# Kernel optimization log

Measured on AMD Instinct MI355X. Metric: run time of the kernel, lower is better.

The kernel has to match this reference:

```python
import jax, jax.numpy as jnp
import numpy as np

N = 10000       # atoms
E = 160000      # edges
F = 128         # node_dim
NB = 20         # num radial basis
BLOCKS = 3      # action_blocks
CUTOFF = 5.0
ZMAX = 100
EPS = 1e-8


def _layernorm(x, g, b):
    mu = jnp.mean(x, axis=-1, keepdims=True)
    var = jnp.var(x, axis=-1, keepdims=True)
    return (x - mu) * jax.lax.rsqrt(var + 1e-5) * g + b


def setup_inputs() -> dict:
    key = jax.random.key(0)
    ks = jax.random.split(key, 16)
    W = 0.05  # weight init scale, keeps activations stable over 3 blocks
    inp = {
        "pos": jax.random.uniform(ks[0], (N, 3), dtype=jnp.float32),
        "z": jax.random.randint(ks[1], (N,), 0, ZMAX),
        "edge_index": jax.random.randint(ks[2], (2, E), 0, N),
        "z_embed": jax.random.normal(ks[3], (ZMAX, F), dtype=jnp.float32),
        "Wrbf": jax.random.normal(ks[4], (BLOCKS, NB, 3 * F), dtype=jnp.float32) * W,
        "brbf": jnp.zeros((BLOCKS, 3 * F), jnp.float32),
        "ln_g": jnp.ones((BLOCKS, F), jnp.float32),
        "ln_b": jnp.zeros((BLOCKS, F), jnp.float32),
        "Wm1": jax.random.normal(ks[5], (BLOCKS, F, F), dtype=jnp.float32) * W,
        "bm1": jnp.zeros((BLOCKS, F), jnp.float32),
        "Wm2": jax.random.normal(ks[6], (BLOCKS, F, 3 * F), dtype=jnp.float32) * W,
        "bm2": jnp.zeros((BLOCKS, 3 * F), jnp.float32),
        "Uw": jax.random.normal(ks[7], (BLOCKS, F, F), dtype=jnp.float32) * W,
        "Vw": jax.random.normal(ks[8], (BLOCKS, F, F), dtype=jnp.float32) * W,
        "ln2_g": jnp.ones((BLOCKS, F), jnp.float32),
        "ln2_b": jnp.zeros((BLOCKS, F), jnp.float32),
        "Wu1": jax.random.normal(ks[9], (BLOCKS, 2 * F, F), dtype=jnp.float32) * W,
        "bu1": jnp.zeros((BLOCKS, F), jnp.float32),
        "Wu2": jax.random.normal(ks[10], (BLOCKS, F, 3 * F), dtype=jnp.float32) * W,
        "bu2": jnp.zeros((BLOCKS, 3 * F), jnp.float32),
        "Wo1": jax.random.normal(ks[11], (F, F), dtype=jnp.float32) * W,
        "bo1": jnp.zeros((F,), jnp.float32),
        "Wo2": jax.random.normal(ks[12], (F, 1), dtype=jnp.float32) * W,
        "bo2": jnp.zeros((1,), jnp.float32),
    }
    return inp


def _forward(pos, z, edge_index, z_embed, Wrbf, brbf, ln_g, ln_b, Wm1, bm1,
             Wm2, bm2, Uw, Vw, ln2_g, ln2_b, Wu1, bu1, Wu2, bu2,
             Wo1, bo1, Wo2, bo2):
    src, dst = edge_index[0], edge_index[1]
    # ---- edge data: distances, bessel RBF, cosine cutoff ----
    rvec = pos[dst] - pos[src]                          # [E,3]
    d = jnp.sqrt(jnp.sum(rvec * rvec, axis=-1) + EPS)   # [E]
    rhat = rvec / d[:, None]                            # [E,3]
    n = jnp.arange(1, NB + 1, dtype=jnp.float32)
    rbf = jnp.sin(n[None, :] * jnp.pi * d[:, None] / CUTOFF) / d[:, None]  # [E,NB]
    fc = jnp.where(d < CUTOFF, 0.5 * (jnp.cos(jnp.pi * d / CUTOFF) + 1.0), 0.0)
    # ---- embedding ----
    x = z_embed[z]                                      # [N,F] scalar features
    v = jnp.zeros((x.shape[0], 3, F), x.dtype)          # [N,3,F] vector features
    nseg = x.shape[0]
    for b in range(BLOCKS):
        # ---- message block (PaiNN) ----
        xn = _layernorm(x, ln_g[b], ln_b[b])
        phi = jax.nn.silu(xn @ Wm1[b] + bm1[b]) @ Wm2[b] + bm2[b]          # [N,3F]
        Wf = (rbf @ Wrbf[b] + brbf[b]) * fc[:, None]                       # [E,3F]
        m = phi[src] * Wf                                                  # [E,3F]
        ms, mvv, mvs = m[:, :F], m[:, F:2 * F], m[:, 2 * F:]
        dx = jax.ops.segment_sum(ms, dst, num_segments=nseg)               # [N,F]
        ev = mvv[:, None, :] * v[src] + mvs[:, None, :] * rhat[:, :, None] # [E,3,F]
        dv = jax.ops.segment_sum(ev, dst, num_segments=nseg)               # [N,3,F]
        x = x + dx
        v = v + dv
        # ---- update block (PaiNN) ----
        Uv = jnp.einsum('ncf,fg->ncg', v, Uw[b])
        Vv = jnp.einsum('ncf,fg->ncg', v, Vw[b])
        vnorm = jnp.sqrt(jnp.sum(Vv * Vv, axis=1) + EPS)                   # [N,F]
        xn2 = _layernorm(x, ln2_g[b], ln2_b[b])
        a = jax.nn.silu(jnp.concatenate([xn2, vnorm], -1) @ Wu1[b] + bu1[b]) @ Wu2[b] + bu2[b]
        avv, asv, ass = a[:, :F], a[:, F:2 * F], a[:, 2 * F:]
        x = x + asv * jnp.sum(Uv * Vv, axis=1) + ass
        v = v + avv[:, None, :] * Uv
    # ---- energy output head ----
    e_atom = jax.nn.silu(x @ Wo1 + bo1) @ Wo2 + bo2                        # [N,1]
    return jnp.sum(e_atom)


def reference(pos, z, edge_index, z_embed, Wrbf, brbf, ln_g, ln_b, Wm1, bm1,
              Wm2, bm2, Uw, Vw, ln2_g, ln2_b, Wu1, bu1, Wu2, bu2,
              Wo1, bo1, Wo2, bo2):
    return _forward(pos, z, edge_index, z_embed, Wrbf, brbf, ln_g, ln_b,
                    Wm1, bm1, Wm2, bm2, Uw, Vw, ln2_g, ln2_b,
                    Wu1, bu1, Wu2, bu2, Wo1, bo1, Wo2, bo2)
```

## Files before the change

kernel.cpp:

```cpp
#include <hip/hip_runtime.h>
#include <math.h>

#define N_ATOM 10000
#define NEDGE  160000
#define F      128
#define F3     384
#define NB     20
#define NBLK   3
#define PI_F   3.14159265358979323846f

typedef __attribute__((ext_vector_type(8))) short bf16x8;
typedef __attribute__((ext_vector_type(4))) float f32x4;
#define MFMA16(a,b,c) __builtin_amdgcn_mfma_f32_16x16x32_bf16(a,b,c,0,0,0)

__device__ __forceinline__ float silu_f(float x){ return x / (1.0f + __expf(-x)); }
__device__ __forceinline__ short f2b(float f){
  unsigned u = __float_as_uint(f);
  u += 0x7fff + ((u >> 16) & 1);
  return (short)(u >> 16);
}
__device__ __forceinline__ float b2f(short s){
  return __uint_as_float(((unsigned)(unsigned short)s) << 16);
}

__global__ __launch_bounds__(256) void k_prep(const float* __restrict__ Wm1, const float* __restrict__ Wm2,
                                              const float* __restrict__ Uw,  const float* __restrict__ Vw,
                                              const float* __restrict__ Wu1, const float* __restrict__ Wu2,
                                              short* __restrict__ wt){
  int idx = blockIdx.x * 256 + threadIdx.x;
  short* wm1t = wt;
  short* wm2t = wt + 49152;
  short* uwt  = wt + 196608;
  short* vwt  = wt + 245760;
  short* wu1t = wt + 294912;
  short* wu2t = wt + 393216;
  if (idx < 49152){
    int b = idx >> 14, r = idx & 16383, n = r >> 7, k = r & 127;
    wm1t[idx] = f2b(Wm1[b*16384 + k*128 + n]);
  } else if (idx < 196608){
    int j = idx - 49152;
    int b = j / 49152, r = j % 49152, n = r >> 7, k = r & 127;
    wm2t[j] = f2b(Wm2[b*49152 + k*384 + n]);
  } else if (idx < 245760){
    int j = idx - 196608;
    int b = j >> 14, r = j & 16383, n = r >> 7, k = r & 127;
    uwt[j] = f2b(Uw[b*16384 + k*128 + n]);
  } else if (idx < 294912){
    int j = idx - 245760;
    int b = j >> 14, r = j & 16383, n = r >> 7, k = r & 127;
    vwt[j] = f2b(Vw[b*16384 + k*128 + n]);
  } else if (idx < 393216){
    int j = idx - 294912;
    int b = j >> 15, r = j & 32767, n = r >> 8, k = r & 255;
    wu1t[j] = f2b(Wu1[b*32768 + k*128 + n]);
  } else if (idx < 540672){
    int j = idx - 393216;
    int b = j / 49152, r = j % 49152, n = r >> 7, k = r & 127;
    wu2t[j] = f2b(Wu2[b*49152 + k*384 + n]);
  }
}

__global__ __launch_bounds__(256) void k_init(const float* __restrict__ z_embed,
                                              const int* __restrict__ z,
                                              float* __restrict__ x, float* __restrict__ v){
  int idx = blockIdx.x * 256 + threadIdx.x;
  if (idx < N_ATOM * F){
    int i = idx >> 7, f = idx & 127;
    x[idx] = z_embed[z[i] * F + f];
  }
  if (idx < N_ATOM * 3 * F) v[idx] = 0.0f;
}

__global__ __launch_bounds__(256) void k_hist(const int* __restrict__ ei, int* __restrict__ deg){
  int e = blockIdx.x * 256 + threadIdx.x;
  atomicAdd(&deg[ei[NEDGE + e]], 1);
}

__global__ __launch_bounds__(1024) void k_scan(const int* __restrict__ deg,
                                               int* __restrict__ rowptr, int* __restrict__ cursor){
  __shared__ int part[1024];
  int t = threadIdx.x;
  int base = t * 10;
  int loc[10];
  int s = 0;
  #pragma unroll
  for (int i = 0; i < 10; i++){
    int idx = base + i;
    int d = (idx < N_ATOM) ? deg[idx] : 0;
    loc[i] = s; s += d;
  }
  part[t] = s;
  __syncthreads();
  for (int off = 1; off < 1024; off <<= 1){
    int vp = 0;
    if (t >= off) vp = part[t - off];
    __syncthreads();
    part[t] += vp;
    __syncthreads();
  }
  int offset = (t == 0) ? 0 : part[t - 1];
  #pragma unroll
  for (int i = 0; i < 10; i++){
    int idx = base + i;
    if (idx < N_ATOM){ rowptr[idx] = offset + loc[i]; cursor[idx] = offset + loc[i]; }
  }
  if (t == 1023) rowptr[N_ATOM] = part[1023];
}

__global__ __launch_bounds__(256) void k_slot(const int* __restrict__ ei,
                                              int* __restrict__ cursor, int* __restrict__ slot){
  int e = blockIdx.x * 256 + threadIdx.x;
  int p = atomicAdd(&cursor[ei[NEDGE + e]], 1);
  slot[e] = p;
}

__global__ __launch_bounds__(256) void k_geo(const float* __restrict__ pos,
                                             const int* __restrict__ ei,
                                             const int* __restrict__ slot,
                                             int* __restrict__ srcs,
                                             float* __restrict__ rhs,
                                             float* __restrict__ rbfs,
                                             float* __restrict__ fcs){
  int e = blockIdx.x * 256 + threadIdx.x;
  int s = ei[e], d_ = ei[NEDGE + e];
  int p = slot[e];
  float rx = pos[d_*3+0] - pos[s*3+0];
  float ry = pos[d_*3+1] - pos[s*3+1];
  float rz = pos[d_*3+2] - pos[s*3+2];
  float d  = sqrtf(rx*rx + ry*ry + rz*rz + 1e-8f);
  float inv = 1.0f / d;
  srcs[p] = s;
  rhs[p*3+0] = rx*inv; rhs[p*3+1] = ry*inv; rhs[p*3+2] = rz*inv;
  float fcv = (d < 5.0f) ? 0.5f * (cosf(PI_F * d * 0.2f) + 1.0f) : 0.0f;
  fcs[p] = fcv;
  float base = PI_F * d * 0.2f;
  float sc = inv * fcv;
  #pragma unroll
  for (int k = 0; k < NB; k++){
    rbfs[(size_t)p*NB + k] = sinf(base * (float)(k+1)) * sc;
  }
}

__global__ __launch_bounds__(256) void k_node_phi(const float* __restrict__ x,
                                                  float* __restrict__ phi,
                                                  const float* __restrict__ ln_g, const float* __restrict__ ln_b,
                                                  const short* __restrict__ Wm1t, const float* __restrict__ bm1,
                                                  const short* __restrict__ Wm2t, const float* __restrict__ bm2){
  __shared__ short xn_s[64*136];
  __shared__ short h_s [64*136];
  __shared__ float mu_s[64], rs_s[64];
  int t = threadIdx.x;
  int row0 = blockIdx.x * 64; if (row0 > N_ATOM - 64) row0 = N_ATOM - 64;

  {
    int r = t >> 2, q = t & 3;
    const float* xr = x + (size_t)(row0 + r) * F;
    float s = 0.f, ss = 0.f;
    #pragma unroll
    for (int i = 0; i < 32; i++){ float vv = xr[q + 4*i]; s += vv; ss += vv*vv; }
    s += __shfl_xor(s, 1, 64); ss += __shfl_xor(ss, 1, 64);
    s += __shfl_xor(s, 2, 64); ss += __shfl_xor(ss, 2, 64);
    if (q == 0){
      float mu = s * (1.0f/F);
      mu_s[r] = mu; rs_s[r] = rsqrtf(ss * (1.0f/F) - mu*mu + 1e-5f);
    }
  }
  __syncthreads();
  #pragma unroll
  for (int i = 0; i < 32; i++){
    int idx = t + 256*i; int r = idx >> 7, f = idx & 127;
    float vv = x[(size_t)(row0 + r)*F + f];
    xn_s[r*136 + f] = f2b((vv - mu_s[r]) * rs_s[r] * ln_g[f] + ln_b[f]);
  }
  __syncthreads();

  int l = t & 63, w = t >> 6;
  int wr0  = w * 16;
  int arow = wr0 + (l & 15);
  int kof  = (l >> 4) * 8;
  int drow = wr0 + (l >> 4) * 4;

  {
    bf16x8 af[4];
    #pragma unroll
    for (int ks = 0; ks < 4; ks++) af[ks] = *(const bf16x8*)&xn_s[arow*136 + ks*32 + kof];
    #pragma unroll
    for (int ct = 0; ct < 8; ct++){
      int col = ct*16 + (l & 15);
      float bb = bm1[col];
      f32x4 acc = {bb, bb, bb, bb};
      #pragma unroll
      for (int ks = 0; ks < 4; ks++){
        bf16x8 bf = *(const bf16x8*)&Wm1t[col*F + ks*32 + kof];
        acc = MFMA16(af[ks], bf, acc);
      }
      #pragma unroll
      for (int i = 0; i < 4; i++) h_s[(drow + i)*136 + col] = f2b(silu_f(acc[i]));
    }
  }
  __syncthreads();
  {
    bf16x8 af[4];
    #pragma unroll
    for (int ks = 0; ks < 4; ks++) af[ks] = *(const bf16x8*)&h_s[arow*136 + ks*32 + kof];
    #pragma unroll
    for (int ct = 0; ct < 24; ct++){
      int col = ct*16 + (l & 15);
      float bb = bm2[col];
      f32x4 acc = {bb, bb, bb, bb};
      #pragma unroll
      for (int ks = 0; ks < 4; ks++){
        bf16x8 bf = *(const bf16x8*)&Wm2t[col*F + ks*32 + kof];
        acc = MFMA16(af[ks], bf, acc);
      }
      #pragma unroll
      for (int i = 0; i < 4; i++) phi[(size_t)(row0 + drow + i)*F3 + col] = acc[i];
    }
  }
}

__global__ __launch_bounds__(256) void k_edge_g(const int* __restrict__ rowptr,
                                                const int* __restrict__ srcs,
                                                const float* __restrict__ rbfs,
                                                const float* __restrict__ rhs,
                                                const float* __restrict__ fcs,
                                                const float* __restrict__ phi,
                                                const float* __restrict__ v,
                                                const float* __restrict__ Wrbf,
                                                const float* __restrict__ brbf,
                                                float* __restrict__ x,
                                                float* __restrict__ vnew){
  __shared__ float W[NB * F3];
  int t = threadIdx.x;
  #pragma unroll
  for (int i = 0; i < (NB*F3)/256; i++) W[t + 256*i] = Wrbf[t + 256*i];
  __syncthreads();

  int wid = t >> 6, lane = t & 63;
  int n = blockIdx.x * 4 + wid;
  int f0 = lane, f1 = lane + 64;
  int r0 = rowptr[n], r1 = rowptr[n+1];

  float bs0  = brbf[f0],       bs1  = brbf[f1];
  float bvv0 = brbf[F + f0],   bvv1 = brbf[F + f1];
  float bvs0 = brbf[2*F + f0], bvs1 = brbf[2*F + f1];

  float ax0=0.f, ax1=0.f;
  float av00=0.f, av01=0.f, av10=0.f, av11=0.f, av20=0.f, av21=0.f;

  for (int j = r0; j < r1; ++j){
    int s = srcs[j];
    float fcv = fcs[j];
    float rh0 = rhs[j*3+0], rh1 = rhs[j*3+1], rh2 = rhs[j*3+2];
    const float* rb = rbfs + (size_t)j * NB;
    float w_s0=0.f, w_s1=0.f, wvv0=0.f, wvv1=0.f, wvs0=0.f, wvs1=0.f;
    #pragma unroll
    for (int k = 0; k < NB; k++){
      float r = rb[k];
      w_s0 += r * W[k*F3 + f0];        w_s1 += r * W[k*F3 + f1];
      wvv0 += r * W[k*F3 + F + f0];    wvv1 += r * W[k*F3 + F + f1];
      wvs0 += r * W[k*F3 + 2*F + f0];  wvs1 += r * W[k*F3 + 2*F + f1];
    }
    const float* ps = phi + (size_t)s * F3;
    const float* vs = v   + (size_t)s * 3 * F;
    float ms0  = ps[f0]       * (w_s0 + bs0 *fcv);
    float ms1  = ps[f1]       * (w_s1 + bs1 *fcv);
    float mvv0 = ps[F + f0]   * (wvv0 + bvv0*fcv);
    float mvv1 = ps[F + f1]   * (wvv1 + bvv1*fcv);
    float mvs0 = ps[2*F + f0] * (wvs0 + bvs0*fcv);
    float mvs1 = ps[2*F + f1] * (wvs1 + bvs1*fcv);
    ax0 += ms0; ax1 += ms1;
    av00 += mvv0*vs[f0]       + mvs0*rh0;  av01 += mvv1*vs[f1]       + mvs1*rh0;
    av10 += mvv0*vs[F + f0]   + mvs0*rh1;  av11 += mvv1*vs[F + f1]   + mvs1*rh1;
    av20 += mvv0*vs[2*F + f0] + mvs0*rh2;  av21 += mvv1*vs[2*F + f1] + mvs1*rh2;
  }

  size_t xb = (size_t)n * F;
  x[xb + f0] += ax0;  x[xb + f1] += ax1;
  size_t vb = (size_t)n * 3 * F;
  vnew[vb + f0]       = v[vb + f0]       + av00;  vnew[vb + f1]       = v[vb + f1]       + av01;
  vnew[vb + F + f0]   = v[vb + F + f0]   + av10;  vnew[vb + F + f1]   = v[vb + F + f1]   + av11;
  vnew[vb + 2*F + f0] = v[vb + 2*F + f0] + av20;  vnew[vb + 2*F + f1] = v[vb + 2*F + f1] + av21;
}

__global__ __launch_bounds__(256) void k_node_upd(float* __restrict__ x, float* __restrict__ v,
                                                  const float* __restrict__ vnew,
                                                  const short* __restrict__ Uwt, const short* __restrict__ Vwt,
                                                  const float* __restrict__ ln2_g, const float* __restrict__ ln2_b,
                                                  const short* __restrict__ Wu1t, const float* __restrict__ bu1,
                                                  const short* __restrict__ Wu2t, const float* __restrict__ bu2){
  __shared__ __align__(16) char smem[59776];
  short* vt   = (short*)smem;
  short* Uv_s = (short*)(smem + 13056);
  char*  R    = smem + 26112;
  short* Vv_s = (short*)R;
  short* ab   = (short*)(R + 13056);
  float* a_s  = (float*)R;
  short* h2   = (short*)(smem + 50688);
  short* duv  = (short*)(smem + 55040);
  float* mu_s = (float*)(smem + 59392);
  float* rs_s = mu_s + 16;

  int t = threadIdx.x;
  int n0 = blockIdx.x * 16;

  {
    int r = t >> 4, q = t & 15;
    const float* xr = x + (size_t)(n0 + r) * F;
    float s = 0.f, ss = 0.f;
    #pragma unroll
    for (int i = 0; i < 8; i++){ float vv = xr[q + 16*i]; s += vv; ss += vv*vv; }
    #pragma unroll
    for (int m = 8; m >= 1; m >>= 1){ s += __shfl_xor(s, m, 64); ss += __shfl_xor(ss, m, 64); }
    if (q == 0){ float mu = s*(1.0f/F); mu_s[r] = mu; rs_s[r] = rsqrtf(ss*(1.0f/F) - mu*mu + 1e-5f); }
  }
  #pragma unroll
  for (int i = 0; i < 24; i++){
    int idx = t + 256*i; int row = idx >> 7, f = idx & 127;
    vt[row*136 + f] = f2b(vnew[(size_t)(n0*3 + row)*F + f]);
  }
  __syncthreads();

  int l = t & 63, w = t >> 6;
  int kof = (l >> 4) * 8;

  {
    #pragma unroll
    for (int jj = 0; jj < 3; jj++){
      int job = w*3 + jj;
      int rt = job >> 2, rem = job & 3, mat = rem >> 1, ch = rem & 1;
      const short* Bt = mat ? Vwt : Uwt;
      short* Out = mat ? Vv_s : Uv_s;
      bf16x8 af[4];
      #pragma unroll
      for (int ks = 0; ks < 4; ks++) af[ks] = *(const bf16x8*)&vt[(rt*16 + (l&15))*136 + ks*32 + kof];
      #pragma unroll
      for (int ct = 0; ct < 4; ct++){
        int col = ch*64 + ct*16 + (l & 15);
        f32x4 acc = {0.f, 0.f, 0.f, 0.f};
        #pragma unroll
        for (int ks = 0; ks < 4; ks++){
          bf16x8 bf = *(const bf16x8*)&Bt[col*F + ks*32 + kof];
          acc = MFMA16(af[ks], bf, acc);
        }
        #pragma unroll
        for (int i = 0; i < 4; i++) Out[(rt*16 + (l>>4)*4 + i)*136 + col] = f2b(acc[i]);
      }
    }
  }
  __syncthreads();

  {
    #pragma unroll
    for (int i = 0; i < 8; i++){
      int idx = t + 256*i; int n = idx >> 7, f = idx & 127;
      float xv = x[(size_t)(n0 + n)*F + f];
      ab[n*264 + f] = f2b((xv - mu_s[n]) * rs_s[n] * ln2_g[f] + ln2_b[f]);
      float v0 = b2f(Vv_s[(3*n+0)*136 + f]), v1 = b2f(Vv_s[(3*n+1)*136 + f]), v2 = b2f(Vv_s[(3*n+2)*136 + f]);
      float u0 = b2f(Uv_s[(3*n+0)*136 + f]), u1 = b2f(Uv_s[(3*n+1)*136 + f]), u2 = b2f(Uv_s[(3*n+2)*136 + f]);
      ab[n*264 + 128 + f] = f2b(sqrtf(v0*v0 + v1*v1 + v2*v2 + 1e-8f));
      duv[n*136 + f] = f2b(u0*v0 + u1*v1 + u2*v2);
    }
  }
  __syncthreads();

  {
    bf16x8 af[8];
    #pragma unroll
    for (int ks = 0; ks < 8; ks++) af[ks] = *(const bf16x8*)&ab[(l&15)*264 + ks*32 + kof];
    #pragma unroll
    for (int cc = 0; cc < 2; cc++){
      int col = (w*2 + cc)*16 + (l & 15);
      float bb = bu1[col];
      f32x4 acc = {bb, bb, bb, bb};
      #pragma unroll
      for (int ks = 0; ks < 8; ks++){
        bf16x8 bf = *(const bf16x8*)&Wu1t[col*256 + ks*32 + kof];
        acc = MFMA16(af[ks], bf, acc);
      }
      #pragma unroll
      for (int i = 0; i < 4; i++) h2[((l>>4)*4 + i)*136 + col] = f2b(silu_f(acc[i]));
    }
  }
  __syncthreads();

  {
    bf16x8 af[4];
    #pragma unroll
    for (int ks = 0; ks < 4; ks++) af[ks] = *(const bf16x8*)&h2[(l&15)*136 + ks*32 + kof];
    #pragma unroll
    for (int cc = 0; cc < 6; cc++){
      int col = (w*6 + cc)*16 + (l & 15);
      float bb = bu2[col];
      f32x4 acc = {bb, bb, bb, bb};
      #pragma unroll
      for (int ks = 0; ks < 4; ks++){
        bf16x8 bf = *(const bf16x8*)&Wu2t[col*F + ks*32 + kof];
        acc = MFMA16(af[ks], bf, acc);
      }
      #pragma unroll
      for (int i = 0; i < 4; i++) a_s[((l>>4)*4 + i)*384 + col] = acc[i];
    }
  }
  __syncthreads();

  {
    #pragma unroll
    for (int i = 0; i < 8; i++){
      int idx = t + 256*i; int n = idx >> 7, f = idx & 127;
      float avv = a_s[n*384 + f], asv = a_s[n*384 + 128 + f], ass = a_s[n*384 + 256 + f];
      size_t xr_ = (size_t)(n0 + n)*F + f;
      x[xr_] = x[xr_] + asv * b2f(duv[n*136 + f]) + ass;
      #pragma unroll
      for (int c = 0; c < 3; c++){
        size_t vr = (size_t)((n0 + n)*3 + c)*F + f;
        v[vr] = vnew[vr] + avv * b2f(Uv_s[(3*n + c)*136 + f]);
      }
    }
  }
}

__global__ __launch_bounds__(256) void k_out(const float* __restrict__ x,
                                             const float* __restrict__ Wo1, const float* __restrict__ bo1,
                                             const float* __restrict__ Wo2, const float* __restrict__ bo2,
                                             float* __restrict__ out){
  __shared__ float xl[8][F];
  __shared__ float hl[8][F];
  __shared__ float er[8];
  int t = threadIdx.x; int n0 = blockIdx.x * 8;
  #pragma unroll
  for (int i = 0; i < 4; i++){ int idx = t + 256*i; ((float*)xl)[idx] = x[(size_t)n0*F + idx]; }
  __syncthreads();
  { int g = t & 127, grp = t >> 7;
    float acc[4];
    #pragma unroll
    for (int n = 0; n < 4; n++) acc[n] = bo1[g];
    for (int k = 0; k < F; k++){
      float w = Wo1[k*F + g];
      #pragma unroll
      for (int n = 0; n < 4; n++) acc[n] += xl[grp*4+n][k] * w;
    }
    #pragma unroll
    for (int n = 0; n < 4; n++) hl[grp*4+n][g] = silu_f(acc[n]);
  }
  __syncthreads();
  { int r = t >> 5, lq = t & 31;
    float s = 0.f;
    #pragma unroll
    for (int i = 0; i < 4; i++) s += hl[r][lq + 32*i] * Wo2[lq + 32*i];
    #pragma unroll
    for (int m = 16; m >= 1; m >>= 1) s += __shfl_xor(s, m, 64);
    if (lq == 0) er[r] = s + bo2[0];
  }
  __syncthreads();
  if (t == 0){
    float s = 0.f;
    #pragma unroll
    for (int r = 0; r < 8; r++) s += er[r];
    unsafeAtomicAdd(out, s);
  }
}

extern "C" void kernel_launch(void* const* d_in, const int* in_sizes, int n_in,
                              void* d_out, int out_size, void* d_ws, size_t ws_size,
                              hipStream_t stream){
  const float* pos     = (const float*)d_in[0];
  const int*   z       = (const int*)  d_in[1];
  const int*   ei      = (const int*)  d_in[2];
  const float* z_embed = (const float*)d_in[3];
  const float* Wrbf    = (const float*)d_in[4];
  const float* brbf    = (const float*)d_in[5];
  const float* ln_g    = (const float*)d_in[6];
  const float* ln_b    = (const float*)d_in[7];
  const float* Wm1     = (const float*)d_in[8];
  const float* bm1     = (const float*)d_in[9];
  const float* Wm2     = (const float*)d_in[10];
  const float* bm2     = (const float*)d_in[11];
  const float* Uw      = (const float*)d_in[12];
  const float* Vw      = (const float*)d_in[13];
  const float* ln2_g   = (const float*)d_in[14];
  const float* ln2_b   = (const float*)d_in[15];
  const float* Wu1     = (const float*)d_in[16];
  const float* bu1     = (const float*)d_in[17];
  const float* Wu2     = (const float*)d_in[18];
  const float* bu2     = (const float*)d_in[19];
  const float* Wo1     = (const float*)d_in[20];
  const float* bo1     = (const float*)d_in[21];
  const float* Wo2     = (const float*)d_in[22];
  const float* bo2     = (const float*)d_in[23];

  float* ws = (float*)d_ws;
  size_t o = 0;
  float* x     = ws + o; o += (size_t)N_ATOM * F;
  float* v     = ws + o; o += (size_t)N_ATOM * 3 * F;
  float* phi   = ws + o; o += (size_t)N_ATOM * 3 * F;
  float* vnew  = ws + o; o += (size_t)N_ATOM * 3 * F;
  float* rhs   = ws + o; o += (size_t)NEDGE * 3;
  float* rbfs  = ws + o; o += (size_t)NEDGE * NB;
  float* fcs   = ws + o; o += (size_t)NEDGE;
  int*   rowptr= (int*)(ws + o); o += N_ATOM + 16;
  int*   srcs  = (int*)(ws + o); o += NEDGE;
  short* wt    = (short*)(ws + o); o += 270336 + 8;
  int* deg    = (int*)vnew;
  int* cursor = deg + 10240;
  int* slot   = cursor + 10240;

  short* wm1t = wt;
  short* wm2t = wt + 49152;
  short* uwt  = wt + 196608;
  short* vwt  = wt + 245760;
  short* wu1t = wt + 294912;
  short* wu2t = wt + 393216;

  hipMemsetAsync(d_out, 0, sizeof(float), stream);
  hipMemsetAsync(deg, 0, N_ATOM * sizeof(int), stream);
  k_prep<<<2112, 256, 0, stream>>>(Wm1, Wm2, Uw, Vw, Wu1, Wu2, wt);
  k_hist<<<NEDGE/256, 256, 0, stream>>>(ei, deg);
  k_scan<<<1, 1024, 0, stream>>>(deg, rowptr, cursor);
  k_slot<<<NEDGE/256, 256, 0, stream>>>(ei, cursor, slot);
  k_geo <<<NEDGE/256, 256, 0, stream>>>(pos, ei, slot, srcs, rhs, rbfs, fcs);
  k_init<<<(N_ATOM*3*F + 255)/256, 256, 0, stream>>>(z_embed, z, x, v);

  for (int b = 0; b < NBLK; b++){
    k_node_phi<<<157, 256, 0, stream>>>(x, phi,
        ln_g + b*F, ln_b + b*F, wm1t + b*16384, bm1 + b*F,
        wm2t + b*49152, bm2 + b*F3);
    k_edge_g<<<N_ATOM/4, 256, 0, stream>>>(rowptr, srcs, rbfs, rhs, fcs,
        phi, v, Wrbf + (size_t)b*NB*F3, brbf + b*F3, x, vnew);
    k_node_upd<<<N_ATOM/16, 256, 0, stream>>>(x, v, vnew,
        uwt + b*16384, vwt + b*16384,
        ln2_g + b*F, ln2_b + b*F,
        wu1t + b*32768, bu1 + b*F,
        wu2t + b*49152, bu2 + b*F3);
  }
  k_out<<<N_ATOM/8, 256, 0, stream>>>(x, Wo1, bo1, Wo2, bo2, (float*)d_out);
}
```

Baseline: 689.8 us.

## Store phi and v in packed bf16 for edge gather, retile node_phi to 16 rows

The per-edge gathers of phi and v now read bf16-packed copies, with phi written packed straight from the MLP and v packed by a new small kernel each block. This halves the bytes fetched per edge in the gather-bound message kernel. k_node_phi is retiled to 16 rows per block with the waves splitting output columns, giving many more blocks. The message kernel now writes only the delta dv, and the update kernel adds v+dv itself. The cost is an extra pack kernel and bf16 rounding of gathered features.

```diff
diff --git a/kernel.cpp b/kernel.cpp
--- a/kernel.cpp
+++ b/kernel.cpp
@@ -21,6 +21,11 @@
 }
 __device__ __forceinline__ float b2f(short s){
   return __uint_as_float(((unsigned)(unsigned short)s) << 16);
+}
+__device__ __forceinline__ float blo(unsigned u){ return __uint_as_float(u << 16); }
+__device__ __forceinline__ float bhi(unsigned u){ return __uint_as_float(u & 0xffff0000u); }
+__device__ __forceinline__ unsigned packb(float a, float b){
+  return ((unsigned)(unsigned short)f2b(a)) | (((unsigned)(unsigned short)f2b(b)) << 16);
 }
 
 __global__ __launch_bounds__(256) void k_prep(const float* __restrict__ Wm1, const float* __restrict__ Wm2,
@@ -71,6 +76,12 @@
   if (idx < N_ATOM * 3 * F) v[idx] = 0.0f;
 }
 
+__global__ __launch_bounds__(256) void k_packv(const float* __restrict__ v, unsigned* __restrict__ v_b){
+  int idx = blockIdx.x * 256 + threadIdx.x;
+  const float* p = v + (size_t)idx * 2;
+  v_b[idx] = packb(p[0], p[1]);
+}
+
 __global__ __launch_bounds__(256) void k_hist(const int* __restrict__ ei, int* __restrict__ deg){
   int e = blockIdx.x * 256 + threadIdx.x;
   atomicAdd(&deg[ei[NEDGE + e]], 1);
@@ -142,24 +153,24 @@
 }
 
 __global__ __launch_bounds__(256) void k_node_phi(const float* __restrict__ x,
-                                                  float* __restrict__ phi,
+                                                  unsigned* __restrict__ phi_b,
                                                   const float* __restrict__ ln_g, const float* __restrict__ ln_b,
                                                   const short* __restrict__ Wm1t, const float* __restrict__ bm1,
                                                   const short* __restrict__ Wm2t, const float* __restrict__ bm2){
-  __shared__ short xn_s[64*136];
-  __shared__ short h_s [64*136];
-  __shared__ float mu_s[64], rs_s[64];
+  __shared__ short xn_s[16*136];
+  __shared__ short h_s [16*136];
+  __shared__ float mu_s[16], rs_s[16];
   int t = threadIdx.x;
-  int row0 = blockIdx.x * 64; if (row0 > N_ATOM - 64) row0 = N_ATOM - 64;
-
-  {
-    int r = t >> 2, q = t & 3;
+  int row0 = blockIdx.x * 16;
+
+  {
+    int r = t >> 4, q = t & 15;
     const float* xr = x + (size_t)(row0 + r) * F;
     float s = 0.f, ss = 0.f;
     #pragma unroll
-    for (int i = 0; i < 32; i++){ float vv = xr[q + 4*i]; s += vv; ss += vv*vv; }
-    s += __shfl_xor(s, 1, 64); ss += __shfl_xor(ss, 1, 64);
-    s += __shfl_xor(s, 2, 64); ss += __shfl_xor(ss, 2, 64);
+    for (int i = 0; i < 8; i++){ float vv = xr[q + 16*i]; s += vv; ss += vv*vv; }
+    #pragma unroll
+    for (int m = 8; m >= 1; m >>= 1){ s += __shfl_xor(s, m, 64); ss += __shfl_xor(ss, m, 64); }
     if (q == 0){
       float mu = s * (1.0f/F);
       mu_s[r] = mu; rs_s[r] = rsqrtf(ss * (1.0f/F) - mu*mu + 1e-5f);
@@ -167,7 +178,7 @@
   }
   __syncthreads();
   #pragma unroll
-  for (int i = 0; i < 32; i++){
+  for (int i = 0; i < 8; i++){
     int idx = t + 256*i; int r = idx >> 7, f = idx & 127;
     float vv = x[(size_t)(row0 + r)*F + f];
     xn_s[r*136 + f] = f2b((vv - mu_s[r]) * rs_s[r] * ln_g[f] + ln_b[f]);
@@ -175,18 +186,16 @@
   __syncthreads();
 
   int l = t & 63, w = t >> 6;
-  int wr0  = w * 16;
-  int arow = wr0 + (l & 15);
-  int kof  = (l >> 4) * 8;
-  int drow = wr0 + (l >> 4) * 4;
+  int kof = (l >> 4) * 8;
+  int arow = l & 15;
 
   {
     bf16x8 af[4];
     #pragma unroll
     for (int ks = 0; ks < 4; ks++) af[ks] = *(const bf16x8*)&xn_s[arow*136 + ks*32 + kof];
     #pragma unroll
-    for (int ct = 0; ct < 8; ct++){
-      int col = ct*16 + (l & 15);
+    for (int cc = 0; cc < 2; cc++){
+      int col = (w*2 + cc)*16 + (l & 15);
       float bb = bm1[col];
       f32x4 acc = {bb, bb, bb, bb};
       #pragma unroll
@@ -195,26 +204,34 @@
         acc = MFMA16(af[ks], bf, acc);
       }
       #pragma unroll
-      for (int i = 0; i < 4; i++) h_s[(drow + i)*136 + col] = f2b(silu_f(acc[i]));
-    }
-  }
-  __syncthreads();
-  {
-    bf16x8 af[4];
-    #pragma unroll
-    for (int ks = 0; ks < 4; ks++) af[ks] = *(const bf16x8*)&h_s[arow*136 + ks*32 + kof];
-    #pragma unroll
-    for (int ct = 0; ct < 24; ct++){
-      int col = ct*16 + (l & 15);
+      for (int i = 0; i < 4; i++) h_s[((l>>4)*4 + i)*136 + col] = f2b(silu_f(acc[i]));
+    }
+  }
+  __syncthreads();
+  {
+    bf16x8 ah[4];
+    #pragma unroll
+    for (int ks = 0; ks < 4; ks++) ah[ks] = *(const bf16x8*)&h_s[arow*136 + ks*32 + kof];
+    #pragma unroll
+    for (int cc = 0; cc < 6; cc++){
+      int col = (w*6 + cc)*16 + (l & 15);
       float bb = bm2[col];
       f32x4 acc = {bb, bb, bb, bb};
       #pragma unroll
       for (int ks = 0; ks < 4; ks++){
         bf16x8 bf = *(const bf16x8*)&Wm2t[col*F + ks*32 + kof];
-        acc = MFMA16(af[ks], bf, acc);
-      }
-      #pragma unroll
-      for (int i = 0; i < 4; i++) phi[(size_t)(row0 + drow + i)*F3 + col] = acc[i];
+        acc = MFMA16(ah[ks], bf, acc);
+      }
+      #pragma unroll
+      for (int i = 0; i < 4; i++){
+        float val = acc[i];
+        float oth = __shfl_xor(val, 1, 64);
+        if (!(l & 1)){
+          int row = row0 + (l>>4)*4 + i;
+          int seg = col >> 7, cin = col & 127;
+          phi_b[(size_t)row*192 + seg*64 + (cin >> 1)] = packb(val, oth);
+        }
+      }
     }
   }
 }
@@ -224,12 +241,12 @@
                                                 const float* __restrict__ rbfs,
                                                 const float* __restrict__ rhs,
                                                 const float* __restrict__ fcs,
-                                                const float* __restrict__ phi,
-                                                const float* __restrict__ v,
+                                                const unsigned* __restrict__ phi_b,
+                                                const unsigned* __restrict__ v_b,
                                                 const float* __restrict__ Wrbf,
                                                 const float* __restrict__ brbf,
                                                 float* __restrict__ x,
-                                                float* __restrict__ vnew){
+                                                float* __restrict__ dv){
   __shared__ float W[NB * F3];
   int t = threadIdx.x;
   #pragma unroll
@@ -238,53 +255,58 @@
 
   int wid = t >> 6, lane = t & 63;
   int n = blockIdx.x * 4 + wid;
-  int f0 = lane, f1 = lane + 64;
+  int f0 = 2 * lane;
   int r0 = rowptr[n], r1 = rowptr[n+1];
 
-  float bs0  = brbf[f0],       bs1  = brbf[f1];
-  float bvv0 = brbf[F + f0],   bvv1 = brbf[F + f1];
-  float bvs0 = brbf[2*F + f0], bvs1 = brbf[2*F + f1];
+  float2 bs  = *(const float2*)&brbf[f0];
+  float2 bvv = *(const float2*)&brbf[F + f0];
+  float2 bvs = *(const float2*)&brbf[2*F + f0];
 
   float ax0=0.f, ax1=0.f;
   float av00=0.f, av01=0.f, av10=0.f, av11=0.f, av20=0.f, av21=0.f;
 
   for (int j = r0; j < r1; ++j){
     int s = srcs[j];
+    const unsigned* pb = phi_b + (size_t)s * 192 + lane;
+    const unsigned* vb = v_b   + (size_t)s * 192 + lane;
+    unsigned p0 = pb[0], p1 = pb[64], p2 = pb[128];
+    unsigned q0 = vb[0], q1 = vb[64], q2 = vb[128];
     float fcv = fcs[j];
     float rh0 = rhs[j*3+0], rh1 = rhs[j*3+1], rh2 = rhs[j*3+2];
     const float* rb = rbfs + (size_t)j * NB;
-    float w_s0=0.f, w_s1=0.f, wvv0=0.f, wvv1=0.f, wvs0=0.f, wvs1=0.f;
+    float ws0=0.f, ws1=0.f, wv0=0.f, wv1=0.f, wq0=0.f, wq1=0.f;
     #pragma unroll
     for (int k = 0; k < NB; k++){
       float r = rb[k];
-      w_s0 += r * W[k*F3 + f0];        w_s1 += r * W[k*F3 + f1];
-      wvv0 += r * W[k*F3 + F + f0];    wvv1 += r * W[k*F3 + F + f1];
-      wvs0 += r * W[k*F3 + 2*F + f0];  wvs1 += r * W[k*F3 + 2*F + f1];
-    }
-    const float* ps = phi + (size_t)s * F3;
-    const float* vs = v   + (size_t)s * 3 * F;
-    float ms0  = ps[f0]       * (w_s0 + bs0 *fcv);
-    float ms1  = ps[f1]       * (w_s1 + bs1 *fcv);
-    float mvv0 = ps[F + f0]   * (wvv0 + bvv0*fcv);
-    float mvv1 = ps[F + f1]   * (wvv1 + bvv1*fcv);
-    float mvs0 = ps[2*F + f0] * (wvs0 + bvs0*fcv);
-    float mvs1 = ps[2*F + f1] * (wvs1 + bvs1*fcv);
+      float2 w0 = *(const float2*)&W[k*F3 + f0];
+      float2 w1 = *(const float2*)&W[k*F3 + F + f0];
+      float2 w2 = *(const float2*)&W[k*F3 + 2*F + f0];
+      ws0 += r*w0.x; ws1 += r*w0.y;
+      wv0 += r*w1.x; wv1 += r*w1.y;
+      wq0 += r*w2.x; wq1 += r*w2.y;
+    }
+    float ms0  = blo(p0) * (ws0 + bs.x *fcv);
+    float ms1  = bhi(p0) * (ws1 + bs.y *fcv);
+    float mvv0 = blo(p1) * (wv0 + bvv.x*fcv);
+    float mvv1 = bhi(p1) * (wv1 + bvv.y*fcv);
+    float mvs0 = blo(p2) * (wq0 + bvs.x*fcv);
+    float mvs1 = bhi(p2) * (wq1 + bvs.y*fcv);
     ax0 += ms0; ax1 += ms1;
-    av00 += mvv0*vs[f0]       + mvs0*rh0;  av01 += mvv1*vs[f1]       + mvs1*rh0;
-    av10 += mvv0*vs[F + f0]   + mvs0*rh1;  av11 += mvv1*vs[F + f1]   + mvs1*rh1;
-    av20 += mvv0*vs[2*F + f0] + mvs0*rh2;  av21 += mvv1*vs[2*F + f1] + mvs1*rh2;
-  }
-
-  size_t xb = (size_t)n * F;
-  x[xb + f0] += ax0;  x[xb + f1] += ax1;
-  size_t vb = (size_t)n * 3 * F;
-  vnew[vb + f0]       = v[vb + f0]       + av00;  vnew[vb + f1]       = v[vb + f1]       + av01;
-  vnew[vb + F + f0]   = v[vb + F + f0]   + av10;  vnew[vb + F + f1]   = v[vb + F + f1]   + av11;
-  vnew[vb + 2*F + f0] = v[vb + 2*F + f0] + av20;  vnew[vb + 2*F + f1] = v[vb + 2*F + f1] + av21;
+    av00 += mvv0*blo(q0) + mvs0*rh0;  av01 += mvv1*bhi(q0) + mvs1*rh0;
+    av10 += mvv0*blo(q1) + mvs0*rh1;  av11 += mvv1*bhi(q1) + mvs1*rh1;
+    av20 += mvv0*blo(q2) + mvs0*rh2;  av21 += mvv1*bhi(q2) + mvs1*rh2;
+  }
+
+  float2* xp = (float2*)&x[(size_t)n*F + f0];
+  float2 xv = *xp; xv.x += ax0; xv.y += ax1; *xp = xv;
+  size_t vb0 = (size_t)n * 3 * F;
+  *(float2*)&dv[vb0 + f0]       = make_float2(av00, av01);
+  *(float2*)&dv[vb0 + F + f0]   = make_float2(av10, av11);
+  *(float2*)&dv[vb0 + 2*F + f0] = make_float2(av20, av21);
 }
 
 __global__ __launch_bounds__(256) void k_node_upd(float* __restrict__ x, float* __restrict__ v,
-                                                  const float* __restrict__ vnew,
+                                                  const float* __restrict__ dv,
                                                   const short* __restrict__ Uwt, const short* __restrict__ Vwt,
                                                   const float* __restrict__ ln2_g, const float* __restrict__ ln2_b,
                                                   const short* __restrict__ Wu1t, const float* __restrict__ bu1,
@@ -316,8 +338,9 @@
   }
   #pragma unroll
   for (int i = 0; i < 24; i++){
-    int idx = t + 256*i; int row = idx >> 7, f = idx & 127;
-    vt[row*136 + f] = f2b(vnew[(size_t)(n0*3 + row)*F + f]);
+    int idx = t + 256*i;
+    size_t g = (size_t)n0*3*F + idx;
+    vt[(idx >> 7)*136 + (idx & 127)] = f2b(v[g] + dv[g]);
   }
   __syncthreads();
 
@@ -414,7 +437,7 @@
       #pragma unroll
       for (int c = 0; c < 3; c++){
         size_t vr = (size_t)((n0 + n)*3 + c)*F + f;
-        v[vr] = vnew[vr] + avv * b2f(Uv_s[(3*n + c)*136 + f]);
+        v[vr] = v[vr] + dv[vr] + avv * b2f(Uv_s[(3*n + c)*136 + f]);
       }
     }
   }
@@ -491,17 +514,18 @@
 
   float* ws = (float*)d_ws;
   size_t o = 0;
-  float* x     = ws + o; o += (size_t)N_ATOM * F;
-  float* v     = ws + o; o += (size_t)N_ATOM * 3 * F;
-  float* phi   = ws + o; o += (size_t)N_ATOM * 3 * F;
-  float* vnew  = ws + o; o += (size_t)N_ATOM * 3 * F;
-  float* rhs   = ws + o; o += (size_t)NEDGE * 3;
-  float* rbfs  = ws + o; o += (size_t)NEDGE * NB;
-  float* fcs   = ws + o; o += (size_t)NEDGE;
-  int*   rowptr= (int*)(ws + o); o += N_ATOM + 16;
-  int*   srcs  = (int*)(ws + o); o += NEDGE;
-  short* wt    = (short*)(ws + o); o += 270336 + 8;
-  int* deg    = (int*)vnew;
+  float*    x     = ws + o; o += (size_t)N_ATOM * F;
+  float*    v     = ws + o; o += (size_t)N_ATOM * 3 * F;
+  float*    dv    = ws + o; o += (size_t)N_ATOM * 3 * F;
+  unsigned* phi_b = (unsigned*)(ws + o); o += (size_t)N_ATOM * 192;
+  unsigned* v_b   = (unsigned*)(ws + o); o += (size_t)N_ATOM * 192;
+  float*    rhs   = ws + o; o += (size_t)NEDGE * 3;
+  float*    rbfs  = ws + o; o += (size_t)NEDGE * NB;
+  float*    fcs   = ws + o; o += (size_t)NEDGE;
+  int*      rowptr= (int*)(ws + o); o += N_ATOM + 16;
+  int*      srcs  = (int*)(ws + o); o += NEDGE;
+  short*    wt    = (short*)(ws + o); o += 270336 + 8;
+  int* deg    = (int*)dv;
   int* cursor = deg + 10240;
   int* slot   = cursor + 10240;
 
@@ -522,12 +546,13 @@
   k_init<<<(N_ATOM*3*F + 255)/256, 256, 0, stream>>>(z_embed, z, x, v);
 
   for (int b = 0; b < NBLK; b++){
-    k_node_phi<<<157, 256, 0, stream>>>(x, phi,
+    k_node_phi<<<N_ATOM/16, 256, 0, stream>>>(x, phi_b,
         ln_g + b*F, ln_b + b*F, wm1t + b*16384, bm1 + b*F,
         wm2t + b*49152, bm2 + b*F3);
+    k_packv<<<(N_ATOM*192)/256, 256, 0, stream>>>(v, v_b);
     k_edge_g<<<N_ATOM/4, 256, 0, stream>>>(rowptr, srcs, rbfs, rhs, fcs,
-        phi, v, Wrbf + (size_t)b*NB*F3, brbf + b*F3, x, vnew);
-    k_node_upd<<<N_ATOM/16, 256, 0, stream>>>(x, v, vnew,
+        phi_b, v_b, Wrbf + (size_t)b*NB*F3, brbf + b*F3, x, dv);
+    k_node_upd<<<N_ATOM/16, 256, 0, stream>>>(x, v, dv,
         uwt + b*16384, vwt + b*16384,
         ln2_g + b*F, ln2_b + b*F,
         wu1t + b*32768, bu1 + b*F,
```

New measurement: 815.8 us. +18.3%, slower.

## Shrink phi kernel tiles, prefetch edge gathers, store dv delta instead of vnew

Applied to the files above, without the earlier changes.

k_node_phi now processes 16 rows per block instead of 64, giving 625 blocks instead of 157. The four waves split the output columns rather than the rows, which should spread work across more CUs. k_edge_g software-prefetches the next edge's phi, v, rhs and fc values so the gather latency overlaps with the radial-basis FMA work. It also writes only the message delta dv instead of v+dv, which removes a v read per node but adds an extra v read in k_node_upd.

```diff
diff --git a/kernel.cpp b/kernel.cpp
--- a/kernel.cpp
+++ b/kernel.cpp
@@ -146,20 +146,20 @@
                                                   const float* __restrict__ ln_g, const float* __restrict__ ln_b,
                                                   const short* __restrict__ Wm1t, const float* __restrict__ bm1,
                                                   const short* __restrict__ Wm2t, const float* __restrict__ bm2){
-  __shared__ short xn_s[64*136];
-  __shared__ short h_s [64*136];
-  __shared__ float mu_s[64], rs_s[64];
+  __shared__ short xn_s[16*136];
+  __shared__ short h_s [16*136];
+  __shared__ float mu_s[16], rs_s[16];
   int t = threadIdx.x;
-  int row0 = blockIdx.x * 64; if (row0 > N_ATOM - 64) row0 = N_ATOM - 64;
-
-  {
-    int r = t >> 2, q = t & 3;
+  int row0 = blockIdx.x * 16;
+
+  {
+    int r = t >> 4, q = t & 15;
     const float* xr = x + (size_t)(row0 + r) * F;
     float s = 0.f, ss = 0.f;
     #pragma unroll
-    for (int i = 0; i < 32; i++){ float vv = xr[q + 4*i]; s += vv; ss += vv*vv; }
-    s += __shfl_xor(s, 1, 64); ss += __shfl_xor(ss, 1, 64);
-    s += __shfl_xor(s, 2, 64); ss += __shfl_xor(ss, 2, 64);
+    for (int i = 0; i < 8; i++){ float vv = xr[q + 16*i]; s += vv; ss += vv*vv; }
+    #pragma unroll
+    for (int m = 8; m >= 1; m >>= 1){ s += __shfl_xor(s, m, 64); ss += __shfl_xor(ss, m, 64); }
     if (q == 0){
       float mu = s * (1.0f/F);
       mu_s[r] = mu; rs_s[r] = rsqrtf(ss * (1.0f/F) - mu*mu + 1e-5f);
@@ -167,7 +167,7 @@
   }
   __syncthreads();
   #pragma unroll
-  for (int i = 0; i < 32; i++){
+  for (int i = 0; i < 8; i++){
     int idx = t + 256*i; int r = idx >> 7, f = idx & 127;
     float vv = x[(size_t)(row0 + r)*F + f];
     xn_s[r*136 + f] = f2b((vv - mu_s[r]) * rs_s[r] * ln_g[f] + ln_b[f]);
@@ -175,18 +175,16 @@
   __syncthreads();
 
   int l = t & 63, w = t >> 6;
-  int wr0  = w * 16;
-  int arow = wr0 + (l & 15);
-  int kof  = (l >> 4) * 8;
-  int drow = wr0 + (l >> 4) * 4;
+  int kof = (l >> 4) * 8;
+  int arow = l & 15;
 
   {
     bf16x8 af[4];
     #pragma unroll
     for (int ks = 0; ks < 4; ks++) af[ks] = *(const bf16x8*)&xn_s[arow*136 + ks*32 + kof];
     #pragma unroll
-    for (int ct = 0; ct < 8; ct++){
-      int col = ct*16 + (l & 15);
+    for (int cc = 0; cc < 2; cc++){
+      int col = (w*2 + cc)*16 + (l & 15);
       float bb = bm1[col];
       f32x4 acc = {bb, bb, bb, bb};
       #pragma unroll
@@ -195,26 +193,27 @@
         acc = MFMA16(af[ks], bf, acc);
       }
       #pragma unroll
-      for (int i = 0; i < 4; i++) h_s[(drow + i)*136 + col] = f2b(silu_f(acc[i]));
-    }
-  }
-  __syncthreads();
-  {
-    bf16x8 af[4];
-    #pragma unroll
-    for (int ks = 0; ks < 4; ks++) af[ks] = *(const bf16x8*)&h_s[arow*136 + ks*32 + kof];
-    #pragma unroll
-    for (int ct = 0; ct < 24; ct++){
-      int col = ct*16 + (l & 15);
+      for (int i = 0; i < 4; i++) h_s[((l>>4)*4 + i)*136 + col] = f2b(silu_f(acc[i]));
+    }
+  }
+  __syncthreads();
+  {
+    bf16x8 ah[4];
+    #pragma unroll
+    for (int ks = 0; ks < 4; ks++) ah[ks] = *(const bf16x8*)&h_s[arow*136 + ks*32 + kof];
+    #pragma unroll
+    for (int cc = 0; cc < 6; cc++){
+      int col = (w*6 + cc)*16 + (l & 15);
       float bb = bm2[col];
       f32x4 acc = {bb, bb, bb, bb};
       #pragma unroll
       for (int ks = 0; ks < 4; ks++){
         bf16x8 bf = *(const bf16x8*)&Wm2t[col*F + ks*32 + kof];
-        acc = MFMA16(af[ks], bf, acc);
+        acc = MFMA16(ah[ks], bf, acc);
       }
       #pragma unroll
-      for (int i = 0; i < 4; i++) phi[(size_t)(row0 + drow + i)*F3 + col] = acc[i];
+      for (int i = 0; i < 4; i++)
+        phi[(size_t)(row0 + (l>>4)*4 + i)*F3 + col] = acc[i];
     }
   }
 }
@@ -229,7 +228,7 @@
                                                 const float* __restrict__ Wrbf,
                                                 const float* __restrict__ brbf,
                                                 float* __restrict__ x,
-                                                float* __restrict__ vnew){
+                                                float* __restrict__ dv){
   __shared__ float W[NB * F3];
   int t = threadIdx.x;
   #pragma unroll
@@ -248,43 +247,59 @@
   float ax0=0.f, ax1=0.f;
   float av00=0.f, av01=0.f, av10=0.f, av11=0.f, av20=0.f, av21=0.f;
 
+  float fcP, rh0P, rh1P, rh2P;
+  float pA, pB, pC, pD, pE, pFv;
+  float vA, vB, vC, vD, vE, vFv;
+  #define PREF(JJ) do{ int s_ = srcs[JJ]; fcP = fcs[JJ]; \
+      rh0P = rhs[(JJ)*3+0]; rh1P = rhs[(JJ)*3+1]; rh2P = rhs[(JJ)*3+2]; \
+      const float* ps_ = phi + (size_t)s_ * F3; \
+      const float* vs_ = v   + (size_t)s_ * 3 * F; \
+      pA = ps_[f0];       pB = ps_[f1]; \
+      pC = ps_[F + f0];   pD = ps_[F + f1]; \
+      pE = ps_[2*F + f0]; pFv = ps_[2*F + f1]; \
+      vA = vs_[f0];       vB = vs_[f1]; \
+      vC = vs_[F + f0];   vD = vs_[F + f1]; \
+      vE = vs_[2*F + f0]; vFv = vs_[2*F + f1]; }while(0)
+
+  if (r0 < r1) PREF(r0);
   for (int j = r0; j < r1; ++j){
-    int s = srcs[j];
-    float fcv = fcs[j];
-    float rh0 = rhs[j*3+0], rh1 = rhs[j*3+1], rh2 = rhs[j*3+2];
+    float fcv = fcP, rh0 = rh0P, rh1 = rh1P, rh2 = rh2P;
+    float pa = pA, pb = pB, pc = pC, pd = pD, pe = pE, pf = pFv;
+    float va = vA, vb = vB, vc = vC, vd = vD, ve = vE, vf = vFv;
+    if (j + 1 < r1) PREF(j + 1);
+
     const float* rb = rbfs + (size_t)j * NB;
-    float w_s0=0.f, w_s1=0.f, wvv0=0.f, wvv1=0.f, wvs0=0.f, wvs1=0.f;
+    float ws0=0.f, ws1=0.f, wv0=0.f, wv1=0.f, wq0=0.f, wq1=0.f;
     #pragma unroll
     for (int k = 0; k < NB; k++){
       float r = rb[k];
-      w_s0 += r * W[k*F3 + f0];        w_s1 += r * W[k*F3 + f1];
-      wvv0 += r * W[k*F3 + F + f0];    wvv1 += r * W[k*F3 + F + f1];
-      wvs0 += r * W[k*F3 + 2*F + f0];  wvs1 += r * W[k*F3 + 2*F + f1];
-    }
-    const float* ps = phi + (size_t)s * F3;
-    const float* vs = v   + (size_t)s * 3 * F;
-    float ms0  = ps[f0]       * (w_s0 + bs0 *fcv);
-    float ms1  = ps[f1]       * (w_s1 + bs1 *fcv);
-    float mvv0 = ps[F + f0]   * (wvv0 + bvv0*fcv);
-    float mvv1 = ps[F + f1]   * (wvv1 + bvv1*fcv);
-    float mvs0 = ps[2*F + f0] * (wvs0 + bvs0*fcv);
-    float mvs1 = ps[2*F + f1] * (wvs1 + bvs1*fcv);
+      ws0 += r * W[k*F3 + f0];        ws1 += r * W[k*F3 + f1];
+      wv0 += r * W[k*F3 + F + f0];    wv1 += r * W[k*F3 + F + f1];
+      wq0 += r * W[k*F3 + 2*F + f0];  wq1 += r * W[k*F3 + 2*F + f1];
+    }
+    float ms0  = pa * (ws0 + bs0 *fcv);
+    float ms1  = pb * (ws1 + bs1 *fcv);
+    float mvv0 = pc * (wv0 + bvv0*fcv);
+    float mvv1 = pd * (wv1 + bvv1*fcv);
+    float mvs0 = pe * (wq0 + bvs0*fcv);
+    float mvs1 = pf * (wq1 + bvs1*fcv);
     ax0 += ms0; ax1 += ms1;
-    av00 += mvv0*vs[f0]       + mvs0*rh0;  av01 += mvv1*vs[f1]       + mvs1*rh0;
-    av10 += mvv0*vs[F + f0]   + mvs0*rh1;  av11 += mvv1*vs[F + f1]   + mvs1*rh1;
-    av20 += mvv0*vs[2*F + f0] + mvs0*rh2;  av21 += mvv1*vs[2*F + f1] + mvs1*rh2;
-  }
+    av00 += mvv0*va + mvs0*rh0;  av01 += mvv1*vb + mvs1*rh0;
+    av10 += mvv0*vc + mvs0*rh1;  av11 += mvv1*vd + mvs1*rh1;
+    av20 += mvv0*ve + mvs0*rh2;  av21 += mvv1*vf + mvs1*rh2;
+  }
+  #undef PREF
 
   size_t xb = (size_t)n * F;
   x[xb + f0] += ax0;  x[xb + f1] += ax1;
-  size_t vb = (size_t)n * 3 * F;
-  vnew[vb + f0]       = v[vb + f0]       + av00;  vnew[vb + f1]       = v[vb + f1]       + av01;
-  vnew[vb + F + f0]   = v[vb + F + f0]   + av10;  vnew[vb + F + f1]   = v[vb + F + f1]   + av11;
-  vnew[vb + 2*F + f0] = v[vb + 2*F + f0] + av20;  vnew[vb + 2*F + f1] = v[vb + 2*F + f1] + av21;
+  size_t vb0 = (size_t)n * 3 * F;
+  dv[vb0 + f0]       = av00;  dv[vb0 + f1]       = av01;
+  dv[vb0 + F + f0]   = av10;  dv[vb0 + F + f1]   = av11;
+  dv[vb0 + 2*F + f0] = av20;  dv[vb0 + 2*F + f1] = av21;
 }
 
 __global__ __launch_bounds__(256) void k_node_upd(float* __restrict__ x, float* __restrict__ v,
-                                                  const float* __restrict__ vnew,
+                                                  const float* __restrict__ dv,
                                                   const short* __restrict__ Uwt, const short* __restrict__ Vwt,
                                                   const float* __restrict__ ln2_g, const float* __restrict__ ln2_b,
                                                   const short* __restrict__ Wu1t, const float* __restrict__ bu1,
@@ -316,8 +331,9 @@
   }
   #pragma unroll
   for (int i = 0; i < 24; i++){
-    int idx = t + 256*i; int row = idx >> 7, f = idx & 127;
-    vt[row*136 + f] = f2b(vnew[(size_t)(n0*3 + row)*F + f]);
+    int idx = t + 256*i;
+    size_t g = (size_t)n0*3*F + idx;
+    vt[(idx >> 7)*136 + (idx & 127)] = f2b(v[g] + dv[g]);
   }
   __syncthreads();
 
@@ -414,7 +430,7 @@
       #pragma unroll
       for (int c = 0; c < 3; c++){
         size_t vr = (size_t)((n0 + n)*3 + c)*F + f;
-        v[vr] = vnew[vr] + avv * b2f(Uv_s[(3*n + c)*136 + f]);
+        v[vr] = v[vr] + dv[vr] + avv * b2f(Uv_s[(3*n + c)*136 + f]);
       }
     }
   }
@@ -493,15 +509,15 @@
   size_t o = 0;
   float* x     = ws + o; o += (size_t)N_ATOM * F;
   float* v     = ws + o; o += (size_t)N_ATOM * 3 * F;
+  float* dv    = ws + o; o += (size_t)N_ATOM * 3 * F;
   float* phi   = ws + o; o += (size_t)N_ATOM * 3 * F;
-  float* vnew  = ws + o; o += (size_t)N_ATOM * 3 * F;
   float* rhs   = ws + o; o += (size_t)NEDGE * 3;
   float* rbfs  = ws + o; o += (size_t)NEDGE * NB;
   float* fcs   = ws + o; o += (size_t)NEDGE;
   int*   rowptr= (int*)(ws + o); o += N_ATOM + 16;
   int*   srcs  = (int*)(ws + o); o += NEDGE;
   short* wt    = (short*)(ws + o); o += 270336 + 8;
-  int* deg    = (int*)vnew;
+  int* deg    = (int*)dv;
   int* cursor = deg + 10240;
   int* slot   = cursor + 10240;
 
@@ -522,12 +538,12 @@
   k_init<<<(N_ATOM*3*F + 255)/256, 256, 0, stream>>>(z_embed, z, x, v);
 
   for (int b = 0; b < NBLK; b++){
-    k_node_phi<<<157, 256, 0, stream>>>(x, phi,
+    k_node_phi<<<N_ATOM/16, 256, 0, stream>>>(x, phi,
         ln_g + b*F, ln_b + b*F, wm1t + b*16384, bm1 + b*F,
         wm2t + b*49152, bm2 + b*F3);
     k_edge_g<<<N_ATOM/4, 256, 0, stream>>>(rowptr, srcs, rbfs, rhs, fcs,
-        phi, v, Wrbf + (size_t)b*NB*F3, brbf + b*F3, x, vnew);
-    k_node_upd<<<N_ATOM/16, 256, 0, stream>>>(x, v, vnew,
+        phi, v, Wrbf + (size_t)b*NB*F3, brbf + b*F3, x, dv);
+    k_node_upd<<<N_ATOM/16, 256, 0, stream>>>(x, v, dv,
         uwt + b*16384, vwt + b*16384,
         ln2_g + b*F, ln2_b + b*F,
         wu1t + b*32768, bu1 + b*F,
```

Result: slower. 712.7 us (+3.3%).
